# Kernel optimization log

Hardware: AMD Instinct MI355X
Metric: run time of the kernel (lower is better)

Reference implementation:

```python
import jax, jax.numpy as jnp
import numpy as np

B, S = 4, 4096
VOCAB = 32000
HIDDEN = 2048
INT_DIM = 64
N_LC = 8192


def _gelu(x):
    # torch nn.GELU() default is the exact (erf) formulation
    return jax.nn.gelu(x, approximate=False)


def setup_inputs() -> dict:
    key = jax.random.key(0)
    ks = jax.random.split(key, 12)
    inp = {
        "input_ids": jax.random.randint(ks[0], (B, S), 0, VOCAB, dtype=jnp.int64) if jax.config.jax_enable_x64 else jax.random.randint(ks[0], (B, S), 0, VOCAB, dtype=jnp.int32),
        "lc_values": jax.random.normal(ks[1], (N_LC, 1), dtype=jnp.float32),
        "pos_b": jax.random.randint(ks[2], (N_LC,), 0, B, dtype=jnp.int32),
        "pos_s": jax.random.randint(ks[3], (N_LC,), 0, S, dtype=jnp.int32),
        # learned params
        "wte": jax.random.normal(ks[4], (VOCAB, HIDDEN), dtype=jnp.float32) * 0.02,
        "W0": jax.random.normal(ks[5], (1, INT_DIM), dtype=jnp.float32) * 0.5,
        "b0": jnp.zeros((INT_DIM,), dtype=jnp.float32),
        "W1": jax.random.normal(ks[6], (INT_DIM, INT_DIM), dtype=jnp.float32) * (1.0 / np.sqrt(INT_DIM)),
        "b1": jnp.zeros((INT_DIM,), dtype=jnp.float32),
        "W2": jax.random.normal(ks[7], (INT_DIM, INT_DIM), dtype=jnp.float32) * (1.0 / np.sqrt(INT_DIM)),
        "b2": jnp.zeros((INT_DIM,), dtype=jnp.float32),
        "Wout": jax.random.normal(ks[8], (INT_DIM, HIDDEN), dtype=jnp.float32) * (1.0 / np.sqrt(INT_DIM)),
        "bout": jnp.zeros((HIDDEN,), dtype=jnp.float32),
    }
    return inp


def reference(input_ids, lc_values, pos_b, pos_s, wte, W0, b0, W1, b1, W2, b2, Wout, bout):
    V = wte.shape[0]
    # clamp_min(0).clamp_max(vocab_size); clip to V-1 so the gather is in-range
    ids = jnp.clip(input_ids, 0, V - 1)
    hidden = wte[ids]  # [B, S, H] embedding gather
    h = lc_values @ W0 + b0
    h = _gelu(h) @ W1 + b1
    h = _gelu(h) @ W2 + b2
    lc_features = _gelu(h) @ Wout + bout  # [N_lc, H]
    # index_put(..., accumulate=False): overwrite rows at (pos_b, pos_s)
    return hidden.at[pos_b, pos_s].set(lc_features.astype(hidden.dtype))
```

## Files before the change

kernel.cpp:

```cpp
#include <hip/hip_runtime.h>
#include <hip/hip_bf16.h>
#include <math.h>

#define BB 4
#define SS 4096
#define HH 2048
#define VOCAB 32000
#define NLC 8192
#define ROWS (BB*SS)
#define RPB 32

__device__ __forceinline__ float gelu_exact(float x) {
    return 0.5f * x * (1.0f + erff(x * 0.70710678118654752f));
}

__global__ void scatter_win_kernel(const int* __restrict__ pos_b, const int* __restrict__ pos_s,
                                   int* __restrict__ win) {
    int i = blockIdx.x * blockDim.x + threadIdx.x;
    if (i < NLC) {
        int p = pos_b[i] * SS + pos_s[i];
        atomicMax(&win[p], i + 1);
    }
}

__global__ void mlp_g2_kernel(const float* __restrict__ lc, const float* __restrict__ W0,
                              const float* __restrict__ b0, const float* __restrict__ W1,
                              const float* __restrict__ b1, const float* __restrict__ W2,
                              const float* __restrict__ b2, float* __restrict__ g2out) {
    int w = threadIdx.x >> 6;
    int j = threadIdx.x & 63;
    int row = blockIdx.x * 4 + w;
    __shared__ float g[4][64];
    float x = lc[row];
    float h = gelu_exact(fmaf(x, W0[j], b0[j]));
    g[w][j] = h;
    __syncthreads();
    float acc = b1[j];
#pragma unroll
    for (int k = 0; k < 64; ++k) acc = fmaf(g[w][k], W1[k * 64 + j], acc);
    acc = gelu_exact(acc);
    __syncthreads();
    g[w][j] = acc;
    __syncthreads();
    float acc2 = b2[j];
#pragma unroll
    for (int k = 0; k < 64; ++k) acc2 = fmaf(g[w][k], W2[k * 64 + j], acc2);
    g2out[row * 64 + j] = gelu_exact(acc2);
}

__global__ void feat_scatter_kernel(const float* __restrict__ g2, const int* __restrict__ win,
                                    const int* __restrict__ pos_b, const int* __restrict__ pos_s,
                                    const float* __restrict__ Wout, const float* __restrict__ bout,
                                    float* __restrict__ out) {
    __shared__ float wlds[64][256];
    __shared__ float g2s[RPB][64];
    __shared__ int   wrow[RPB];
    int t = threadIdx.x;
    int base = blockIdx.x * RPB;

    for (int e = t; e < RPB * 64; e += 256) g2s[e >> 6][e & 63] = g2[base * 64 + e];
    if (t < RPB) {
        int i = base + t;
        int p = pos_b[i] * SS + pos_s[i];
        wrow[t] = (win[p] == i + 1) ? p : -1;
    }
    int w = t >> 6, l = t & 63;

    for (int c = 0; c < 8; ++c) {
        __syncthreads();
        for (int e4 = t; e4 < 64 * 64; e4 += 256) {
            int k = e4 >> 6, col4 = e4 & 63;
            *(float4*)&wlds[k][col4 * 4] = *(const float4*)&Wout[k * HH + c * 256 + col4 * 4];
        }
        __syncthreads();
        for (int rg = 0; rg < RPB / 4; ++rg) {
            int r = rg * 4 + w;
            int p = wrow[r];
            if (p < 0) continue;
            float4 acc = *(const float4*)&bout[c * 256 + l * 4];
#pragma unroll
            for (int k = 0; k < 64; ++k) {
                float gk = g2s[r][k];
                float4 wv = *(const float4*)&wlds[k][l * 4];
                acc.x = fmaf(gk, wv.x, acc.x);
                acc.y = fmaf(gk, wv.y, acc.y);
                acc.z = fmaf(gk, wv.z, acc.z);
                acc.w = fmaf(gk, wv.w, acc.w);
            }
            *(float4*)&out[(size_t)p * HH + c * 256 + l * 4] = acc;
        }
    }
}

__global__ void gather_kernel(const int* __restrict__ ids, const int* __restrict__ win,
                              const float* __restrict__ wte, float* __restrict__ out) {
    int row = blockIdx.x;
    if (win[row] != 0) return;
    int id = ids[row];
    id = id < 0 ? 0 : (id > VOCAB - 1 ? VOCAB - 1 : id);
    const float4* src = (const float4*)(wte + (size_t)id * HH);
    float4* dst = (float4*)(out + (size_t)row * HH);
    for (int e = threadIdx.x; e < HH / 4; e += 256) dst[e] = src[e];
}

extern "C" void kernel_launch(void* const* d_in, const int* in_sizes, int n_in,
                              void* d_out, int out_size, void* d_ws, size_t ws_size,
                              hipStream_t stream) {
    const int*   ids  = (const int*)d_in[0];
    const float* lc   = (const float*)d_in[1];
    const int*   pb   = (const int*)d_in[2];
    const int*   ps   = (const int*)d_in[3];
    const float* wte  = (const float*)d_in[4];
    const float* W0   = (const float*)d_in[5];
    const float* b0   = (const float*)d_in[6];
    const float* W1   = (const float*)d_in[7];
    const float* b1   = (const float*)d_in[8];
    const float* W2   = (const float*)d_in[9];
    const float* b2   = (const float*)d_in[10];
    const float* Wout = (const float*)d_in[11];
    const float* bout = (const float*)d_in[12];
    float* out = (float*)d_out;

    int*   win = (int*)d_ws;
    float* g2  = (float*)((char*)d_ws + ROWS * sizeof(int));

    hipMemsetAsync(win, 0, ROWS * sizeof(int), stream);
    scatter_win_kernel<<<NLC / 256, 256, 0, stream>>>(pb, ps, win);
    mlp_g2_kernel<<<NLC / 4, 256, 0, stream>>>(lc, W0, b0, W1, b1, W2, b2, g2);
    feat_scatter_kernel<<<NLC / RPB, 256, 0, stream>>>(g2, win, pb, ps, Wout, bout, out);
    gather_kernel<<<ROWS, 256, 0, stream>>>(ids, win, wte, out);
}
```

Before: 489.1 us.

## Register-tile Wout projection and split columns across blocks

The output projection kernel no longer stages a 64x256 Wout slab in LDS across eight column passes. Each block now handles 32 rows by 512 columns, reading Wout straight from global/L2 into registers and keeping 8x8 float4 accumulators per thread. The grid grows from 256 to 1024 blocks for more parallelism, and the per-chunk LDS syncs go away. The costs are higher register pressure and redundant Wout reads from global, and rows that lose the scatter still spend compute.

```diff
diff --git a/kernel.cpp b/kernel.cpp
--- a/kernel.cpp
+++ b/kernel.cpp
@@ -8,7 +8,9 @@
 #define VOCAB 32000
 #define NLC 8192
 #define ROWS (BB*SS)
-#define RPB 32
+
+#define FROWS 32
+#define FCOLS 512
 
 __device__ __forceinline__ float gelu_exact(float x) {
     return 0.5f * x * (1.0f + erff(x * 0.70710678118654752f));
@@ -52,43 +54,68 @@
                                     const int* __restrict__ pos_b, const int* __restrict__ pos_s,
                                     const float* __restrict__ Wout, const float* __restrict__ bout,
                                     float* __restrict__ out) {
-    __shared__ float wlds[64][256];
-    __shared__ float g2s[RPB][64];
-    __shared__ int   wrow[RPB];
+    __shared__ float g2s[FROWS][64];
+    __shared__ int   wrow[FROWS];
     int t = threadIdx.x;
-    int base = blockIdx.x * RPB;
+    int rblk = blockIdx.x & 255;
+    int cb   = (blockIdx.x >> 8) * FCOLS;
+    int base = rblk * FROWS;
 
-    for (int e = t; e < RPB * 64; e += 256) g2s[e >> 6][e & 63] = g2[base * 64 + e];
-    if (t < RPB) {
+    {
+        const float4* src = (const float4*)(g2 + base * 64);
+        float4* dst = (float4*)&g2s[0][0];
+        dst[t] = src[t];
+        dst[t + 256] = src[t + 256];
+    }
+    if (t < FROWS) {
         int i = base + t;
         int p = pos_b[i] * SS + pos_s[i];
         wrow[t] = (win[p] == i + 1) ? p : -1;
     }
+    __syncthreads();
+
     int w = t >> 6, l = t & 63;
+    const float* wbase = Wout + cb + l * 4;
 
-    for (int c = 0; c < 8; ++c) {
-        __syncthreads();
-        for (int e4 = t; e4 < 64 * 64; e4 += 256) {
-            int k = e4 >> 6, col4 = e4 & 63;
-            *(float4*)&wlds[k][col4 * 4] = *(const float4*)&Wout[k * HH + c * 256 + col4 * 4];
+    float4 bv0 = *(const float4*)&bout[cb + l * 4];
+    float4 bv1 = *(const float4*)&bout[cb + 256 + l * 4];
+    float4 acc0[8], acc1[8];
+#pragma unroll
+    for (int r = 0; r < 8; ++r) { acc0[r] = bv0; acc1[r] = bv1; }
+
+    for (int k0 = 0; k0 < 64; k0 += 4) {
+        float4 wv0[4], wv1[4];
+#pragma unroll
+        for (int kk = 0; kk < 4; ++kk) {
+            const float* wp = wbase + (size_t)(k0 + kk) * HH;
+            wv0[kk] = *(const float4*)wp;
+            wv1[kk] = *(const float4*)(wp + 256);
         }
-        __syncthreads();
-        for (int rg = 0; rg < RPB / 4; ++rg) {
-            int r = rg * 4 + w;
-            int p = wrow[r];
-            if (p < 0) continue;
-            float4 acc = *(const float4*)&bout[c * 256 + l * 4];
 #pragma unroll
-            for (int k = 0; k < 64; ++k) {
-                float gk = g2s[r][k];
-                float4 wv = *(const float4*)&wlds[k][l * 4];
-                acc.x = fmaf(gk, wv.x, acc.x);
-                acc.y = fmaf(gk, wv.y, acc.y);
-                acc.z = fmaf(gk, wv.z, acc.z);
-                acc.w = fmaf(gk, wv.w, acc.w);
+        for (int r = 0; r < 8; ++r) {
+            float4 gv = *(const float4*)&g2s[w * 8 + r][k0];
+#pragma unroll
+            for (int c = 0; c < 4; ++c) {
+                float g0 = (&gv.x)[0], g1 = (&gv.x)[1], g2v = (&gv.x)[2], g3 = (&gv.x)[3];
+                (&acc0[r].x)[c] = fmaf(g0, (&wv0[0].x)[c],
+                                  fmaf(g1, (&wv0[1].x)[c],
+                                  fmaf(g2v, (&wv0[2].x)[c],
+                                  fmaf(g3, (&wv0[3].x)[c], (&acc0[r].x)[c]))));
+                (&acc1[r].x)[c] = fmaf(g0, (&wv1[0].x)[c],
+                                  fmaf(g1, (&wv1[1].x)[c],
+                                  fmaf(g2v, (&wv1[2].x)[c],
+                                  fmaf(g3, (&wv1[3].x)[c], (&acc1[r].x)[c]))));
             }
-            *(float4*)&out[(size_t)p * HH + c * 256 + l * 4] = acc;
         }
+    }
+
+#pragma unroll
+    for (int r = 0; r < 8; ++r) {
+        int p = wrow[w * 8 + r];
+        if (p < 0) continue;
+        float* op = out + (size_t)p * HH + cb + l * 4;
+        *(float4*)op = acc0[r];
+        *(float4*)(op + 256) = acc1[r];
     }
 }
 
@@ -127,6 +154,6 @@
     hipMemsetAsync(win, 0, ROWS * sizeof(int), stream);
     scatter_win_kernel<<<NLC / 256, 256, 0, stream>>>(pb, ps, win);
     mlp_g2_kernel<<<NLC / 4, 256, 0, stream>>>(lc, W0, b0, W1, b1, W2, b2, g2);
-    feat_scatter_kernel<<<NLC / RPB, 256, 0, stream>>>(g2, win, pb, ps, Wout, bout, out);
+    feat_scatter_kernel<<<(NLC / FROWS) * (HH / FCOLS), 256, 0, stream>>>(g2, win, pb, ps, Wout, bout, out);
     gather_kernel<<<ROWS, 256, 0, stream>>>(ids, win, wte, out);
 }
```

Result: faster. 422.7 us (-13.6%).
